# Optimization experiments

Hardware: AMD Instinct MI355X
Metric: run time of the kernel (lower is better)

## Reference

```python
import jax, jax.numpy as jnp
import numpy as np

B, T, H, L = 8, 256, 64, 3
NB, NF, HP = 17, 68, 6
K = 9  # temporal kernel
PAD = (K - 1) // 2
EPS = 1e-5


def _normalize(adj):
    adj = adj + np.eye(adj.shape[0], dtype=np.float32)
    d = adj.sum(1)
    dinv = np.power(d, -0.5)
    dinv[np.isinf(dinv)] = 0.0
    return (dinv[:, None] * adj * dinv[None, :]).astype(np.float32)


def _body_adj():
    a = np.zeros((NB, NB), np.float32)
    conns = [(0, 1), (0, 2), (1, 3), (2, 4), (0, 5), (0, 6), (5, 6), (5, 7), (7, 9), (6, 8), (8, 10), (5, 11), (6, 12), (11, 12), (11, 13), (13, 15), (12, 14), (14, 16)]
    for i, j in conns:
        a[i, j] = 1.0
        a[j, i] = 1.0
    return _normalize(a)


def _face_adj():
    a = np.zeros((NF, NF), np.float32)
    for i in range(16): a[i, i + 1] = 1.0
    for i in range(17, 21): a[i, i + 1] = 1.0
    for i in range(22, 26): a[i, i + 1] = 1.0
    for i in range(27, 30): a[i, i + 1] = 1.0
    for i in range(31, 35): a[i, i + 1] = 1.0
    for i in range(36, 41): a[i, i + 1] = 1.0
    a[41, 36] = 1.0
    for i in range(42, 47): a[i, i + 1] = 1.0
    a[47, 42] = 1.0
    for i in range(48, 59): a[i, i + 1] = 1.0
    a[59, 48] = 1.0
    for i in range(60, 67): a[i, i + 1] = 1.0
    a[67, 60] = 1.0
    a = a + a.T
    return _normalize(a)


def setup_inputs() -> dict:
    keys = iter(jax.random.split(jax.random.key(0), 80))

    def rn(shape, s):
        return jax.random.normal(next(keys), shape, jnp.float32) * s

    inp = {}
    inp['body_kps'] = jax.random.normal(next(keys), (B, T, NB * 2), jnp.float32)
    inp['face_kps_2d'] = jax.random.normal(next(keys), (B, T, NF * 2), jnp.float32)
    inp['head_pose'] = jax.random.normal(next(keys), (B, T, HP), jnp.float32)
    inp['body_adj'] = jnp.asarray(_body_adj())
    inp['face_adj'] = jnp.asarray(_face_adj())
    inp['body_proj_w'] = rn((2, H), 0.5)
    inp['body_proj_b'] = jnp.zeros((H,), jnp.float32)
    inp['face_proj_w'] = rn((2, H), 0.5)
    inp['face_proj_b'] = jnp.zeros((H,), jnp.float32)
    inp['head_w'] = rn((HP, H), 0.3)
    inp['head_b'] = jnp.zeros((H,), jnp.float32)
    for p in ('b', 'f'):
        inp[p + '_t1w'] = rn((L, H, H, K), 0.04)
        inp[p + '_t1b'] = jnp.zeros((L, H), jnp.float32)
        inp[p + '_bn1g'] = jnp.ones((L, H), jnp.float32)
        inp[p + '_bn1b'] = jnp.zeros((L, H), jnp.float32)
        inp[p + '_bn1m'] = rn((L, H), 0.1)
        inp[p + '_bn1v'] = jax.random.uniform(next(keys), (L, H), jnp.float32, 0.5, 1.5)
        inp[p + '_gcw'] = rn((L, H, H), 0.1)
        inp[p + '_gcb'] = jnp.zeros((L, H), jnp.float32)
        inp[p + '_t2w'] = rn((L, H, H, K), 0.04)
        inp[p + '_t2b'] = jnp.zeros((L, H), jnp.float32)
        inp[p + '_bn2g'] = jnp.ones((L, H), jnp.float32)
        inp[p + '_bn2b'] = jnp.zeros((L, H), jnp.float32)
        inp[p + '_bn2m'] = rn((L, H), 0.1)
        inp[p + '_bn2v'] = jax.random.uniform(next(keys), (L, H), jnp.float32, 0.5, 1.5)
    total = NB * H + NF * H + H  # 5504
    inp['fus1_w'] = rn((total, 4 * H), 0.02)
    inp['fus1_b'] = jnp.zeros((4 * H,), jnp.float32)
    inp['fus2_w'] = rn((4 * H, 2 * H), 0.06)
    inp['fus2_b'] = jnp.zeros((2 * H,), jnp.float32)
    inp['fus3_w'] = rn((2 * H, H), 0.09)
    inp['fus3_b'] = jnp.zeros((H,), jnp.float32)
    inp['fus4_w'] = rn((H, 5), 0.12)
    inp['fus4_b'] = jnp.zeros((5,), jnp.float32)
    return inp


def _conv_bn(x, w, b, g, be, m, v):
    # x: (BN, C, T); w: (O, I, K). Conv1d (pad=4) + eval-mode BatchNorm1d.
    y = jax.lax.conv_general_dilated(x, w, (1,), [(PAD, PAD)], dimension_numbers=('NCH', 'OIH', 'NCH'))
    y = y + b[None, :, None]
    inv = g * jax.lax.rsqrt(v + EPS)
    return y * inv[None, :, None] + (be - m * inv)[None, :, None]


def _block(x, adj, t1w, t1b, g1, b1, m1, v1, gw, gb, t2w, t2b, g2, b2, m2, v2):
    # x: (B, N, C, T); residual is identity (in_channels == out_channels)
    Bn, N, C, Tn = x.shape
    res = x
    h = jax.nn.relu(_conv_bn(x.reshape(Bn * N, C, Tn), t1w, t1b, g1, b1, m1, v1)).reshape(Bn, N, C, Tn)
    # spatial graph conv, batched over all timesteps at once (adj @ (x W) + b)
    support = jnp.einsum('bnct,co->bnot', h, gw)
    h = jax.nn.relu(jnp.einsum('mn,bnot->bmot', adj, support) + gb[None, None, :, None])
    h = _conv_bn(h.reshape(Bn * N, C, Tn), t2w, t2b, g2, b2, m2, v2).reshape(Bn, N, C, Tn)
    return h + res  # dropout = identity in eval


def _stream(x, n_nodes, pw, pb, adj, ps):
    Bn, Tn, _ = x.shape
    h = x.reshape(Bn, Tn, n_nodes, 2) @ pw + pb          # (B, T, N, H)
    h = jnp.transpose(h, (0, 2, 3, 1))                   # (B, N, H, T)
    for l in range(ps[0].shape[0]):
        h = _block(h, adj, *(p[l] for p in ps))
    return h.mean(axis=3).reshape(Bn, -1)                # temporal mean-pool, flatten nodes


def reference(body_kps, face_kps_2d, head_pose, body_adj, face_adj, body_proj_w, body_proj_b, face_proj_w, face_proj_b, head_w, head_b, b_t1w, b_t1b, b_bn1g, b_bn1b, b_bn1m, b_bn1v, b_gcw, b_gcb, b_t2w, b_t2b, b_bn2g, b_bn2b, b_bn2m, b_bn2v, f_t1w, f_t1b, f_bn1g, f_bn1b, f_bn1m, f_bn1v, f_gcw, f_gcb, f_t2w, f_t2b, f_bn2g, f_bn2b, f_bn2m, f_bn2v, fus1_w, fus1_b, fus2_w, fus2_b, fus3_w, fus3_b, fus4_w, fus4_b):
    bps = (b_t1w, b_t1b, b_bn1g, b_bn1b, b_bn1m, b_bn1v, b_gcw, b_gcb, b_t2w, b_t2b, b_bn2g, b_bn2b, b_bn2m, b_bn2v)
    fps = (f_t1w, f_t1b, f_bn1g, f_bn1b, f_bn1m, f_bn1v, f_gcw, f_gcb, f_t2w, f_t2b, f_bn2g, f_bn2b, f_bn2m, f_bn2v)
    bf = _stream(body_kps, NB, body_proj_w, body_proj_b, body_adj, bps)
    ff = _stream(face_kps_2d, NF, face_proj_w, face_proj_b, face_adj, fps)
    hp = jax.nn.relu(head_pose @ head_w + head_b).mean(axis=1)
    feat = jnp.concatenate([bf, ff, hp], axis=-1)
    h = jax.nn.relu(feat @ fus1_w + fus1_b)
    h = jax.nn.relu(h @ fus2_w + fus2_b)
    h = jax.nn.relu(h @ fus3_w + fus3_b)
    return h @ fus4_w + fus4_b
```

## Files before the change

kernel.cpp:

```cpp
#include <hip/hip_runtime.h>

constexpr int B_ = 8, T_ = 256, H_ = 64, L_ = 3, NB_ = 17, NF_ = 68, HP_ = 6, K_ = 9;
constexpr int FEAT_DIM = NB_ * H_ + NF_ * H_ + H_;
constexpr int HT = H_ * T_;

typedef _Float16 half4_t __attribute__((ext_vector_type(4)));
typedef _Float16 half8_t __attribute__((ext_vector_type(8)));
typedef float f32x16 __attribute__((ext_vector_type(16)));
typedef float f32x4 __attribute__((ext_vector_type(4)));

constexpr size_t SZ_AB = (size_t)B_ * NB_ * HT;
constexpr size_t SZ_AF = (size_t)B_ * NF_ * HT;
constexpr size_t OFF_TB   = 0;
constexpr size_t OFF_TF   = OFF_TB + SZ_AB / 2;
constexpr size_t OFF_SUPB = OFF_TF + SZ_AF / 2;
constexpr size_t OFF_SUPF = OFF_SUPB + SZ_AB / 2;
constexpr size_t OFF_GB   = OFF_SUPF + SZ_AF / 2;
constexpr size_t OFF_GF   = OFF_GB + SZ_AB / 2;
constexpr size_t OFF_W3   = OFF_GF + SZ_AF / 2;
constexpr size_t OFF_GW3  = OFF_W3 + 4 * 55296;
constexpr size_t OFF_B2   = OFF_GW3 + 2 * 6144;
constexpr size_t OFF_ADJPB= OFF_B2 + 768;
constexpr size_t OFF_ADJPF= OFF_ADJPB + 512;
constexpr size_t OFF_FEAT = OFF_ADJPF + 3840;
constexpr size_t OFF_P1   = OFF_FEAT + (size_t)B_ * FEAT_DIM;

struct ConvPrepSet { const float *w, *tb, *g, *bb, *m, *v; };

__global__ __launch_bounds__(256) void prep_convW_all(ConvPrepSet s0, ConvPrepSet s1,
                                                      ConvPrepSet s2, ConvPrepSet s3,
                                                      _Float16* __restrict__ w3,
                                                      float* __restrict__ b2) {
    int set = blockIdx.y;
    ConvPrepSet s = (set == 0) ? s0 : (set == 1) ? s1 : (set == 2) ? s2 : s3;
    int idx = blockIdx.x * 256 + threadIdx.x;
    int k = idx % K_; int r = idx / K_;
    int i = r % H_; r /= H_;
    int o = r % H_; int l = r / H_;
    float sc = s.g[l * H_ + o] * rsqrtf(s.v[l * H_ + o] + 1e-5f);
    w3[(size_t)set * 110592 + ((((l * K_ + k) * 8 + (i >> 3)) * H_ + o) * 8) + (i & 7)]
        = (_Float16)(s.w[idx] * sc);
    if (i == 0 && k == 0)
        b2[set * 192 + l * H_ + o] =
            s.tb[l * H_ + o] * sc + s.bb[l * H_ + o] - s.m[l * H_ + o] * sc;
}

__global__ __launch_bounds__(256) void prep_gcw_all(const float* __restrict__ g0,
                                                    const float* __restrict__ g1,
                                                    _Float16* __restrict__ w3) {
    int set = blockIdx.y;
    const float* gw = set ? g1 : g0;
    int idx = blockIdx.x * 256 + threadIdx.x;
    int o = idx % H_; int r = idx / H_;
    int c = r % H_; int l = r / H_;
    w3[(size_t)set * 12288 + (((l * 8 + (c >> 3)) * H_ + o) * 8) + (c & 7)] = (_Float16)gw[idx];
}

__global__ __launch_bounds__(256) void prep_misc(const float* __restrict__ adjB,
                                                 const float* __restrict__ adjF,
                                                 _Float16* __restrict__ pB,
                                                 _Float16* __restrict__ pF,
                                                 float* __restrict__ p1,
                                                 float* __restrict__ feat) {
    int idx = blockIdx.x * 256 + threadIdx.x;
    if (idx < 1024) {
        int m = idx >> 5, k = idx & 31;
        pB[idx] = (m < NB_ && k < NB_) ? (_Float16)adjB[m * NB_ + k] : (_Float16)0.f;
    } else if (idx < 8704) {
        int j = idx - 1024;
        int m = j / 80, k = j % 80;
        pF[j] = (m < NF_ && k < NF_) ? (_Float16)adjF[m * NF_ + k] : (_Float16)0.f;
    } else if (idx < 10752) {
        p1[idx - 8704] = 0.f;
    } else if (idx < 10752 + B_ * FEAT_DIM) {
        feat[idx - 10752] = 0.f;
    }
}

__global__ __launch_bounds__(256) void proj_kernel(const float* __restrict__ kpsB,
                                                   const float* __restrict__ pwB,
                                                   const float* __restrict__ pbB,
                                                   _Float16* __restrict__ outB,
                                                   const float* __restrict__ kpsF,
                                                   const float* __restrict__ pwF,
                                                   const float* __restrict__ pbF,
                                                   _Float16* __restrict__ outF,
                                                   const float* __restrict__ hx,
                                                   const float* __restrict__ hw,
                                                   const float* __restrict__ hb,
                                                   float* __restrict__ feat,
                                                   int nblk0, int nblk1) {
    int blk = blockIdx.x;
    if (blk >= nblk1) {
        int b = blk - nblk1;
        int c = threadIdx.x;
        if (c >= 64) return;
        float w0 = hw[c], w1 = hw[64 + c], w2 = hw[128 + c],
              w3 = hw[192 + c], w4 = hw[256 + c], w5 = hw[320 + c];
        float bias = hb[c];
        float acc = 0.f;
        for (int t = 0; t < T_; ++t) {
            const float* xr = hx + ((size_t)b * T_ + t) * HP_;
            float s = fmaf(xr[0], w0, fmaf(xr[1], w1, fmaf(xr[2], w2,
                      fmaf(xr[3], w3, fmaf(xr[4], w4, fmaf(xr[5], w5, bias))))));
            acc += fmaxf(s, 0.f);
        }
        feat[(size_t)b * FEAT_DIM + NB_ * H_ + NF_ * H_ + c] = acc * (1.f / 256.f);
        return;
    }
    const float *kps, *pw, *pb; _Float16* out; int N, bn;
    if (blk < nblk0) { kps = kpsB; pw = pwB; pb = pbB; out = outB; N = NB_; bn = blk; }
    else { kps = kpsF; pw = pwF; pb = pbF; out = outF; N = NF_; bn = blk - nblk0; }
    int b = bn / N, n = bn % N;
    int t = threadIdx.x;
    float x0 = kps[((size_t)b * T_ + t) * (N * 2) + n * 2 + 0];
    float x1 = kps[((size_t)b * T_ + t) * (N * 2) + n * 2 + 1];
    _Float16* ob = out + (size_t)bn * HT + t;
#pragma unroll 8
    for (int c = 0; c < H_; ++c)
        ob[(size_t)c * T_] = (_Float16)fmaf(x0, pw[c], fmaf(x1, pw[H_ + c], pb[c]));
}

__device__ __forceinline__ half8_t ld_b8(const _Float16* p) {
    half4_t lo = *(const half4_t*)p;
    half4_t hi = *(const half4_t*)(p + 4);
    return __builtin_shufflevector(lo, hi, 0, 1, 2, 3, 4, 5, 6, 7);
}

__device__ __forceinline__ void stage_f16(const _Float16* __restrict__ xb,
                                          _Float16* __restrict__ Xs, int tc, int tid) {
    for (int u = tid; u < 8 * 136; u += 256) {
        int oct = u / 136;
        int row = u - oct * 136;
        int t = tc * 128 + row - 4;
        _Float16 v[8];
        if (t >= 0 && t < T_) {
            const _Float16* xr = xb + (size_t)(oct * 8) * T_ + t;
#pragma unroll
            for (int j = 0; j < 8; ++j) v[j] = xr[(size_t)j * T_];
        } else {
#pragma unroll
            for (int j = 0; j < 8; ++j) v[j] = (_Float16)0.f;
        }
        _Float16* dst = &Xs[row * 68 + oct * 8];
        half4_t lo, hi;
#pragma unroll
        for (int j = 0; j < 4; ++j) { lo[j] = v[j]; hi[j] = v[4 + j]; }
        *(half4_t*)dst = lo;
        *(half4_t*)(dst + 4) = hi;
    }
}

struct CM {
    const _Float16* x; const half8_t* w1; const float* b1; const half8_t* gc; _Float16* sup;
};

__global__ __launch_bounds__(256) void convmix_kernel(CM P0, CM P1, int nblk0, int l) {
    __shared__ __align__(16) _Float16 Xs[136 * 68];
    int blk = blockIdx.x;
    CM P = (blk < nblk0) ? P0 : P1;
    if (blk >= nblk0) blk -= nblk0;
    int bn = blk >> 1, tc = blk & 1;
    int tid = threadIdx.x;
    stage_f16(P.x + (size_t)bn * HT, Xs, tc, tid);
    __syncthreads();

    int ln = tid & 63;
    int w = __builtin_amdgcn_readfirstlane(tid >> 6);
    int ln31 = ln & 31, kg = ln >> 5;
    int tsub = w * 32;

    f32x16 acc[2];
#pragma unroll
    for (int mt = 0; mt < 2; ++mt)
#pragma unroll
        for (int r = 0; r < 16; ++r) acc[mt][r] = 0.f;

    const half8_t* wl = P.w1 + (size_t)l * (K_ * 8 * H_);
    const _Float16* xrow0 = Xs + (size_t)(tsub + ln31) * 68;
#pragma unroll
    for (int tap = 0; tap < K_; ++tap) {
#pragma unroll
        for (int ks = 0; ks < 4; ++ks) {
            int i8 = ks * 2 + kg;
            half8_t a0 = wl[(tap * 8 + i8) * H_ + ln31];
            half8_t a1 = wl[(tap * 8 + i8) * H_ + 32 + ln31];
            half8_t bf = ld_b8(xrow0 + tap * 68 + i8 * 8);
            acc[0] = __builtin_amdgcn_mfma_f32_32x32x16_f16(a0, bf, acc[0], 0, 0, 0);
            acc[1] = __builtin_amdgcn_mfma_f32_32x32x16_f16(a1, bf, acc[1], 0, 0, 0);
        }
    }
    __syncthreads();

    {
        _Float16* mrow = Xs + (size_t)(4 + tsub + ln31) * 68;
#pragma unroll
        for (int mt = 0; mt < 2; ++mt) {
#pragma unroll
            for (int rg = 0; rg < 4; ++rg) {
                int o0 = mt * 32 + rg * 8 + kg * 4;
                f32x4 bv = *(const f32x4*)(P.b1 + l * H_ + o0);
                half4_t hv;
#pragma unroll
                for (int j = 0; j < 4; ++j)
                    hv[j] = (_Float16)fmaxf(acc[mt][rg * 4 + j] + bv[j], 0.f);
                *(half4_t*)(mrow + o0) = hv;
            }
        }
    }
    __syncthreads();

    f32x16 acc2[2];
#pragma unroll
    for (int mt = 0; mt < 2; ++mt)
#pragma unroll
        for (int r = 0; r < 16; ++r) acc2[mt][r] = 0.f;
    const half8_t* gl = P.gc + (size_t)l * (8 * H_);
    const _Float16* mrow = Xs + (size_t)(4 + tsub + ln31) * 68;
#pragma unroll
    for (int ks = 0; ks < 4; ++ks) {
        int i8 = ks * 2 + kg;
        half8_t a0 = gl[i8 * H_ + ln31];
        half8_t a1 = gl[i8 * H_ + 32 + ln31];
        half8_t bf = ld_b8(mrow + i8 * 8);
        acc2[0] = __builtin_amdgcn_mfma_f32_32x32x16_f16(a0, bf, acc2[0], 0, 0, 0);
        acc2[1] = __builtin_amdgcn_mfma_f32_32x32x16_f16(a1, bf, acc2[1], 0, 0, 0);
    }

    int t = tc * 128 + tsub + ln31;
    _Float16* sp = P.sup + (size_t)bn * HT + t;
#pragma unroll
    for (int mt = 0; mt < 2; ++mt) {
#pragma unroll
        for (int r = 0; r < 16; ++r) {
            int o = mt * 32 + (r & 3) + 8 * (r >> 2) + 4 * kg;
            sp[(size_t)o * T_] = (_Float16)acc2[mt][r];
        }
    }
}

struct C2 {
    const _Float16* x; const half8_t* w2; const float* b2; _Float16* trunk; int N; int fbase;
};

template <bool LAST>
__global__ __launch_bounds__(256) void conv2_kernel(C2 P0, C2 P1, int nblk0, int l,
                                                    float* __restrict__ feat) {
    __shared__ __align__(16) _Float16 Xs[136 * 68];
    int blk = blockIdx.x;
    C2 P = (blk < nblk0) ? P0 : P1;
    if (blk >= nblk0) blk -= nblk0;
    int bn = blk >> 1, tc = blk & 1;
    int tid = threadIdx.x;
    stage_f16(P.x + (size_t)bn * HT, Xs, tc, tid);
    __syncthreads();

    int ln = tid & 63;
    int w = __builtin_amdgcn_readfirstlane(tid >> 6);
    int ln31 = ln & 31, kg = ln >> 5;
    int tsub = w * 32;

    f32x16 acc[2];
#pragma unroll
    for (int mt = 0; mt < 2; ++mt)
#pragma unroll
        for (int r = 0; r < 16; ++r) acc[mt][r] = 0.f;

    const half8_t* wl = P.w2 + (size_t)l * (K_ * 8 * H_);
    const _Float16* xrow0 = Xs + (size_t)(tsub + ln31) * 68;
#pragma unroll
    for (int tap = 0; tap < K_; ++tap) {
#pragma unroll
        for (int ks = 0; ks < 4; ++ks) {
            int i8 = ks * 2 + kg;
            half8_t a0 = wl[(tap * 8 + i8) * H_ + ln31];
            half8_t a1 = wl[(tap * 8 + i8) * H_ + 32 + ln31];
            half8_t bf = ld_b8(xrow0 + tap * 68 + i8 * 8);
            acc[0] = __builtin_amdgcn_mfma_f32_32x32x16_f16(a0, bf, acc[0], 0, 0, 0);
            acc[1] = __builtin_amdgcn_mfma_f32_32x32x16_f16(a1, bf, acc[1], 0, 0, 0);
        }
    }

    int t = tc * 128 + tsub + ln31;
    const _Float16* resb = P.trunk + (size_t)bn * HT + t;
    if (!LAST) {
        _Float16* tob = P.trunk + (size_t)bn * HT + t;
#pragma unroll
        for (int mt = 0; mt < 2; ++mt) {
#pragma unroll
            for (int r = 0; r < 16; ++r) {
                int o = mt * 32 + (r & 3) + 8 * (r >> 2) + 4 * kg;
                float y = acc[mt][r] + P.b2[l * H_ + o] + (float)resb[(size_t)o * T_];
                tob[(size_t)o * T_] = (_Float16)y;
            }
        }
    } else {
        __syncthreads();
        float* red = (float*)Xs;
        float sv[2][16];
#pragma unroll
        for (int mt = 0; mt < 2; ++mt) {
#pragma unroll
            for (int r = 0; r < 16; ++r) {
                int o = mt * 32 + (r & 3) + 8 * (r >> 2) + 4 * kg;
                float s = acc[mt][r] + P.b2[l * H_ + o] + (float)resb[(size_t)o * T_];
#pragma unroll
                for (int off = 1; off < 32; off <<= 1) s += __shfl_xor(s, off);
                sv[mt][r] = s;
            }
        }
        if (ln31 == 0) {
#pragma unroll
            for (int mt = 0; mt < 2; ++mt)
#pragma unroll
                for (int r = 0; r < 16; ++r) {
                    int o = mt * 32 + (r & 3) + 8 * (r >> 2) + 4 * kg;
                    red[w * 64 + o] = sv[mt][r];
                }
        }
        __syncthreads();
        if (tid < 64) {
            float s = red[tid] + red[64 + tid] + red[128 + tid] + red[192 + tid];
            int b = bn / P.N, n = bn % P.N;
            atomicAdd(&feat[(size_t)b * FEAT_DIM + P.fbase + n * H_ + tid], s * (1.f / 256.f));
        }
    }
}

template <int N, int MT, int KS>
__device__ __forceinline__ void adjmix_impl(const _Float16* __restrict__ sup,
                                            const half8_t* __restrict__ adjP,
                                            const float* __restrict__ gb,
                                            _Float16* __restrict__ out,
                                            int blk, int l, _Float16* Ls, int tid) {
    constexpr int KP = KS * 16;
    constexpr int PITCH = KP + 4;
    int b = blk >> 7, cb = blk & 127;
    int colbase = cb * 128;
    float gbv = gb[l * H_ + (cb >> 1)];

    for (int u = tid; u < KP * 16; u += 256) {
        int n = u >> 4, cs = u & 15;
        half8_t v;
        if (n < N) v = *(const half8_t*)(sup + (size_t)(b * N + n) * HT + colbase + cs * 8);
        else {
#pragma unroll
            for (int j = 0; j < 8; ++j) v[j] = (_Float16)0.f;
        }
#pragma unroll
        for (int j = 0; j < 8; ++j) Ls[(cs * 8 + j) * PITCH + n] = v[j];
    }
    __syncthreads();

    int ln = tid & 63;
    int w = __builtin_amdgcn_readfirstlane(tid >> 6);
    int ln31 = ln & 31, kg = ln >> 5;
    int colL = w * 32 + ln31;

    f32x16 acc[MT];
#pragma unroll
    for (int mt = 0; mt < MT; ++mt)
#pragma unroll
        for (int r = 0; r < 16; ++r) acc[mt][r] = 0.f;

#pragma unroll
    for (int ks = 0; ks < KS; ++ks) {
        half8_t bf = ld_b8(&Ls[colL * PITCH + ks * 16 + kg * 8]);
#pragma unroll
        for (int mt = 0; mt < MT; ++mt) {
            half8_t af = adjP[(size_t)(mt * 32 + ln31) * (KP / 8) + ks * 2 + kg];
            acc[mt] = __builtin_amdgcn_mfma_f32_32x32x16_f16(af, bf, acc[mt], 0, 0, 0);
        }
    }

    int col = colbase + colL;
#pragma unroll
    for (int mt = 0; mt < MT; ++mt) {
#pragma unroll
        for (int r = 0; r < 16; ++r) {
            int m = mt * 32 + (r & 3) + 8 * (r >> 2) + 4 * kg;
            if (m < N)
                out[(size_t)(b * N + m) * HT + col] = (_Float16)fmaxf(acc[mt][r] + gbv, 0.f);
        }
    }
}

__global__ __launch_bounds__(256) void adjmix_kernel(
        const _Float16* __restrict__ supB, const half8_t* __restrict__ adjPB,
        const float* __restrict__ gbB, _Float16* __restrict__ outB,
        const _Float16* __restrict__ supF, const half8_t* __restrict__ adjPF,
        const float* __restrict__ gbF, _Float16* __restrict__ outF,
        int nblk0, int l) {
    __shared__ __align__(16) _Float16 Ls[128 * 84];
    int blk = blockIdx.x, tid = threadIdx.x;
    if (blk < nblk0)
        adjmix_impl<NB_, 1, 2>(supB, adjPB, gbB, outB, blk, l, Ls, tid);
    else
        adjmix_impl<NF_, 3, 5>(supF, adjPF, gbF, outF, blk - nblk0, l, Ls, tid);
}

__global__ __launch_bounds__(256) void fus1_kernel(const float* __restrict__ feat,
                                                   const float* __restrict__ w1,
                                                   float* __restrict__ p1) {
    __shared__ float fv[128];
    int b = blockIdx.x / 43, ic = blockIdx.x % 43;
    int tid = threadIdx.x;
    if (tid < 128) fv[tid] = feat[(size_t)b * FEAT_DIM + ic * 128 + tid];
    __syncthreads();
    const float* wb = w1 + (size_t)(ic * 128) * 256 + tid;
    float acc = 0.f;
#pragma unroll 4
    for (int i = 0; i < 128; ++i)
        acc = fmaf(fv[i], wb[(size_t)i * 256], acc);
    atomicAdd(&p1[b * 256 + tid], acc);
}

__global__ __launch_bounds__(256) void fus_tail_kernel(const float* __restrict__ p1,
        const float* __restrict__ b1, const float* __restrict__ w2, const float* __restrict__ b2,
        const float* __restrict__ w3, const float* __restrict__ b3,
        const float* __restrict__ w4, const float* __restrict__ b4, float* __restrict__ out) {
    __shared__ float s1[256], s2[128], s3[64];
    int b = blockIdx.x, tid = threadIdx.x;
    s1[tid] = fmaxf(p1[b * 256 + tid] + b1[tid], 0.f);
    __syncthreads();
    if (tid < 128) {
        float acc = b2[tid];
        for (int i = 0; i < 256; ++i) acc = fmaf(s1[i], w2[i * 128 + tid], acc);
        s2[tid] = fmaxf(acc, 0.f);
    }
    __syncthreads();
    if (tid < 64) {
        float acc = b3[tid];
        for (int i = 0; i < 128; ++i) acc = fmaf(s2[i], w3[i * 64 + tid], acc);
        s3[tid] = fmaxf(acc, 0.f);
    }
    __syncthreads();
    if (tid < 5) {
        float acc = b4[tid];
        for (int i = 0; i < 64; ++i) acc = fmaf(s3[i], w4[i * 5 + tid], acc);
        out[b * 5 + tid] = acc;
    }
}

extern "C" void kernel_launch(void* const* d_in, const int* in_sizes, int n_in,
                              void* d_out, int out_size, void* d_ws, size_t ws_size,
                              hipStream_t stream) {
    const float* body_kps = (const float*)d_in[0];
    const float* face_kps = (const float*)d_in[1];
    const float* head_pose = (const float*)d_in[2];
    const float* body_adj = (const float*)d_in[3];
    const float* face_adj = (const float*)d_in[4];
    const float* body_pw = (const float*)d_in[5];
    const float* body_pb = (const float*)d_in[6];
    const float* face_pw = (const float*)d_in[7];
    const float* face_pb = (const float*)d_in[8];
    const float* head_w = (const float*)d_in[9];
    const float* head_b = (const float*)d_in[10];
    const float* b_t1w = (const float*)d_in[11]; const float* b_t1b = (const float*)d_in[12];
    const float* b_g1  = (const float*)d_in[13]; const float* b_b1  = (const float*)d_in[14];
    const float* b_m1  = (const float*)d_in[15]; const float* b_v1  = (const float*)d_in[16];
    const float* b_gcw = (const float*)d_in[17]; const float* b_gcb = (const float*)d_in[18];
    const float* b_t2w = (const float*)d_in[19]; const float* b_t2b = (const float*)d_in[20];
    const float* b_g2  = (const float*)d_in[21]; const float* b_b2  = (const float*)d_in[22];
    const float* b_m2  = (const float*)d_in[23]; const float* b_v2  = (const float*)d_in[24];
    const float* f_t1w = (const float*)d_in[25]; const float* f_t1b = (const float*)d_in[26];
    const float* f_g1  = (const float*)d_in[27]; const float* f_b1  = (const float*)d_in[28];
    const float* f_m1  = (const float*)d_in[29]; const float* f_v1  = (const float*)d_in[30];
    const float* f_gcw = (const float*)d_in[31]; const float* f_gcb = (const float*)d_in[32];
    const float* f_t2w = (const float*)d_in[33]; const float* f_t2b = (const float*)d_in[34];
    const float* f_g2  = (const float*)d_in[35]; const float* f_b2  = (const float*)d_in[36];
    const float* f_m2  = (const float*)d_in[37]; const float* f_v2  = (const float*)d_in[38];
    const float* fus1_w = (const float*)d_in[39]; const float* fus1_b = (const float*)d_in[40];
    const float* fus2_w = (const float*)d_in[41]; const float* fus2_b = (const float*)d_in[42];
    const float* fus3_w = (const float*)d_in[43]; const float* fus3_b = (const float*)d_in[44];
    const float* fus4_w = (const float*)d_in[45]; const float* fus4_b = (const float*)d_in[46];

    float* ws = (float*)d_ws;
    _Float16* TrB = (_Float16*)(ws + OFF_TB);
    _Float16* TrF = (_Float16*)(ws + OFF_TF);
    _Float16* SupB = (_Float16*)(ws + OFF_SUPB);
    _Float16* SupF = (_Float16*)(ws + OFF_SUPF);
    _Float16* Gb = (_Float16*)(ws + OFF_GB);
    _Float16* Gf = (_Float16*)(ws + OFF_GF);
    _Float16* W3 = (_Float16*)(ws + OFF_W3);
    _Float16* W3b1 = W3;            _Float16* W3b2 = W3 + 110592;
    _Float16* W3f1 = W3 + 221184;   _Float16* W3f2 = W3 + 331776;
    _Float16* GW3 = (_Float16*)(ws + OFF_GW3);
    _Float16* GW3b = GW3;           _Float16* GW3f = GW3 + 12288;
    float* B2 = ws + OFF_B2;
    float* B2b1 = B2;        float* B2b2 = B2 + 192;
    float* B2f1 = B2 + 384;  float* B2f2 = B2 + 576;
    _Float16* adjPB = (_Float16*)(ws + OFF_ADJPB);
    _Float16* adjPF = (_Float16*)(ws + OFF_ADJPF);
    float* feat = ws + OFF_FEAT;
    float* p1 = ws + OFF_P1;
    float* out = (float*)d_out;

    ConvPrepSet sb1{b_t1w, b_t1b, b_g1, b_b1, b_m1, b_v1};
    ConvPrepSet sb2{b_t2w, b_t2b, b_g2, b_b2, b_m2, b_v2};
    ConvPrepSet sf1{f_t1w, f_t1b, f_g1, f_b1, f_m1, f_v1};
    ConvPrepSet sf2{f_t2w, f_t2b, f_g2, f_b2, f_m2, f_v2};
    prep_convW_all<<<dim3(432, 4), 256, 0, stream>>>(sb1, sb2, sf1, sf2, W3, B2);
    prep_gcw_all<<<dim3(48, 2), 256, 0, stream>>>(b_gcw, f_gcw, GW3);
    prep_misc<<<214, 256, 0, stream>>>(body_adj, face_adj, adjPB, adjPF, p1, feat);

    const int nB = B_ * NB_;
    const int nF = B_ * NF_;
    proj_kernel<<<nB + nF + B_, 256, 0, stream>>>(body_kps, body_pw, body_pb, TrB,
                                                  face_kps, face_pw, face_pb, TrF,
                                                  head_pose, head_w, head_b, feat,
                                                  nB, nB + nF);

    CM cmb{TrB, (const half8_t*)W3b1, B2b1, (const half8_t*)GW3b, SupB};
    CM cmf{TrF, (const half8_t*)W3f1, B2f1, (const half8_t*)GW3f, SupF};
    C2 c2b{Gb, (const half8_t*)W3b2, B2b2, TrB, NB_, 0};
    C2 c2f{Gf, (const half8_t*)W3f2, B2f2, TrF, NF_, NB_ * H_};

    const int gc = (nB + nF) * 2;
    const int n0 = nB * 2;
    const int ga = B_ * 128;

    for (int l = 0; l < L_; ++l) {
        convmix_kernel<<<gc, 256, 0, stream>>>(cmb, cmf, n0, l);
        adjmix_kernel<<<2 * ga, 256, 0, stream>>>(SupB, (const half8_t*)adjPB, b_gcb, Gb,
                                                  SupF, (const half8_t*)adjPF, f_gcb, Gf, ga, l);
        if (l < L_ - 1)
            conv2_kernel<false><<<gc, 256, 0, stream>>>(c2b, c2f, n0, l, feat);
        else
            conv2_kernel<true><<<gc, 256, 0, stream>>>(c2b, c2f, n0, l, feat);
    }

    fus1_kernel<<<B_ * 43, 256, 0, stream>>>(feat, fus1_w, p1);
    fus_tail_kernel<<<B_, 256, 0, stream>>>(p1, fus1_b, fus2_w, fus2_b, fus3_w, fus3_b,
                                            fus4_w, fus4_b, out);
}
```

Measured before the change: 395.8 us.

## Process full time axis per block in conv kernels to reuse weight fragments

Each convmix and conv2 block now covers all 256 time steps of one (batch,node) instead of half. Each wave computes two 32-step tiles, so every loaded weight fragment feeds two MFMAs, and the 4-row halo is staged once per node instead of twice. The cost is twice the LDS per block, more accumulator registers (launch bounds set to 2 blocks per SM), and half as many blocks in the grid, which lowers parallelism.

```diff
diff --git a/kernel.cpp b/kernel.cpp
--- a/kernel.cpp
+++ b/kernel.cpp
@@ -127,12 +127,12 @@
     return __builtin_shufflevector(lo, hi, 0, 1, 2, 3, 4, 5, 6, 7);
 }
 
-__device__ __forceinline__ void stage_f16(const _Float16* __restrict__ xb,
-                                          _Float16* __restrict__ Xs, int tc, int tid) {
-    for (int u = tid; u < 8 * 136; u += 256) {
-        int oct = u / 136;
-        int row = u - oct * 136;
-        int t = tc * 128 + row - 4;
+__device__ __forceinline__ void stage_full(const _Float16* __restrict__ xb,
+                                           _Float16* __restrict__ Xs, int tid) {
+    for (int u = tid; u < 8 * 264; u += 256) {
+        int oct = u / 264;
+        int row = u - oct * 264;
+        int t = row - 4;
         _Float16 v[8];
         if (t >= 0 && t < T_) {
             const _Float16* xr = xb + (size_t)(oct * 8) * T_ + t;
@@ -155,29 +155,31 @@
     const _Float16* x; const half8_t* w1; const float* b1; const half8_t* gc; _Float16* sup;
 };
 
-__global__ __launch_bounds__(256) void convmix_kernel(CM P0, CM P1, int nblk0, int l) {
-    __shared__ __align__(16) _Float16 Xs[136 * 68];
+__global__ __launch_bounds__(256, 2) void convmix_kernel(CM P0, CM P1, int nblk0, int l) {
+    __shared__ __align__(16) _Float16 Xs[264 * 68];
     int blk = blockIdx.x;
     CM P = (blk < nblk0) ? P0 : P1;
     if (blk >= nblk0) blk -= nblk0;
-    int bn = blk >> 1, tc = blk & 1;
+    int bn = blk;
     int tid = threadIdx.x;
-    stage_f16(P.x + (size_t)bn * HT, Xs, tc, tid);
+    stage_full(P.x + (size_t)bn * HT, Xs, tid);
     __syncthreads();
 
     int ln = tid & 63;
     int w = __builtin_amdgcn_readfirstlane(tid >> 6);
     int ln31 = ln & 31, kg = ln >> 5;
-    int tsub = w * 32;
-
-    f32x16 acc[2];
+    int tw = w * 64;
+
+    f32x16 acc[2][2];
 #pragma unroll
     for (int mt = 0; mt < 2; ++mt)
 #pragma unroll
-        for (int r = 0; r < 16; ++r) acc[mt][r] = 0.f;
+        for (int f = 0; f < 2; ++f)
+#pragma unroll
+            for (int r = 0; r < 16; ++r) acc[mt][f][r] = 0.f;
 
     const half8_t* wl = P.w1 + (size_t)l * (K_ * 8 * H_);
-    const _Float16* xrow0 = Xs + (size_t)(tsub + ln31) * 68;
+    const _Float16* xr0 = Xs + (size_t)(tw + ln31) * 68;
 #pragma unroll
     for (int tap = 0; tap < K_; ++tap) {
 #pragma unroll
@@ -185,56 +187,70 @@
             int i8 = ks * 2 + kg;
             half8_t a0 = wl[(tap * 8 + i8) * H_ + ln31];
             half8_t a1 = wl[(tap * 8 + i8) * H_ + 32 + ln31];
-            half8_t bf = ld_b8(xrow0 + tap * 68 + i8 * 8);
-            acc[0] = __builtin_amdgcn_mfma_f32_32x32x16_f16(a0, bf, acc[0], 0, 0, 0);
-            acc[1] = __builtin_amdgcn_mfma_f32_32x32x16_f16(a1, bf, acc[1], 0, 0, 0);
+            half8_t b0 = ld_b8(xr0 + tap * 68 + i8 * 8);
+            half8_t b1 = ld_b8(xr0 + (32 + tap) * 68 + i8 * 8);
+            acc[0][0] = __builtin_amdgcn_mfma_f32_32x32x16_f16(a0, b0, acc[0][0], 0, 0, 0);
+            acc[0][1] = __builtin_amdgcn_mfma_f32_32x32x16_f16(a0, b1, acc[0][1], 0, 0, 0);
+            acc[1][0] = __builtin_amdgcn_mfma_f32_32x32x16_f16(a1, b0, acc[1][0], 0, 0, 0);
+            acc[1][1] = __builtin_amdgcn_mfma_f32_32x32x16_f16(a1, b1, acc[1][1], 0, 0, 0);
         }
     }
     __syncthreads();
 
     {
-        _Float16* mrow = Xs + (size_t)(4 + tsub + ln31) * 68;
-#pragma unroll
-        for (int mt = 0; mt < 2; ++mt) {
-#pragma unroll
-            for (int rg = 0; rg < 4; ++rg) {
-                int o0 = mt * 32 + rg * 8 + kg * 4;
-                f32x4 bv = *(const f32x4*)(P.b1 + l * H_ + o0);
-                half4_t hv;
-#pragma unroll
-                for (int j = 0; j < 4; ++j)
-                    hv[j] = (_Float16)fmaxf(acc[mt][rg * 4 + j] + bv[j], 0.f);
-                *(half4_t*)(mrow + o0) = hv;
+#pragma unroll
+        for (int f = 0; f < 2; ++f) {
+            _Float16* mrow = Xs + (size_t)(4 + tw + f * 32 + ln31) * 68;
+#pragma unroll
+            for (int mt = 0; mt < 2; ++mt) {
+#pragma unroll
+                for (int rg = 0; rg < 4; ++rg) {
+                    int o0 = mt * 32 + rg * 8 + kg * 4;
+                    f32x4 bv = *(const f32x4*)(P.b1 + l * H_ + o0);
+                    half4_t hv;
+#pragma unroll
+                    for (int j = 0; j < 4; ++j)
+                        hv[j] = (_Float16)fmaxf(acc[mt][f][rg * 4 + j] + bv[j], 0.f);
+                    *(half4_t*)(mrow + o0) = hv;
+                }
             }
         }
     }
     __syncthreads();
 
-    f32x16 acc2[2];
+    f32x16 acc2[2][2];
 #pragma unroll
     for (int mt = 0; mt < 2; ++mt)
 #pragma unroll
-        for (int r = 0; r < 16; ++r) acc2[mt][r] = 0.f;
+        for (int f = 0; f < 2; ++f)
+#pragma unroll
+            for (int r = 0; r < 16; ++r) acc2[mt][f][r] = 0.f;
     const half8_t* gl = P.gc + (size_t)l * (8 * H_);
-    const _Float16* mrow = Xs + (size_t)(4 + tsub + ln31) * 68;
+    const _Float16* mrow0 = Xs + (size_t)(4 + tw + ln31) * 68;
 #pragma unroll
     for (int ks = 0; ks < 4; ++ks) {
         int i8 = ks * 2 + kg;
         half8_t a0 = gl[i8 * H_ + ln31];
         half8_t a1 = gl[i8 * H_ + 32 + ln31];
-        half8_t bf = ld_b8(mrow + i8 * 8);
-        acc2[0] = __builtin_amdgcn_mfma_f32_32x32x16_f16(a0, bf, acc2[0], 0, 0, 0);
-        acc2[1] = __builtin_amdgcn_mfma_f32_32x32x16_f16(a1, bf, acc2[1], 0, 0, 0);
-    }
-
-    int t = tc * 128 + tsub + ln31;
-    _Float16* sp = P.sup + (size_t)bn * HT + t;
+        half8_t b0 = ld_b8(mrow0 + i8 * 8);
+        half8_t b1 = ld_b8(mrow0 + 32 * 68 + i8 * 8);
+        acc2[0][0] = __builtin_amdgcn_mfma_f32_32x32x16_f16(a0, b0, acc2[0][0], 0, 0, 0);
+        acc2[0][1] = __builtin_amdgcn_mfma_f32_32x32x16_f16(a0, b1, acc2[0][1], 0, 0, 0);
+        acc2[1][0] = __builtin_amdgcn_mfma_f32_32x32x16_f16(a1, b0, acc2[1][0], 0, 0, 0);
+        acc2[1][1] = __builtin_amdgcn_mfma_f32_32x32x16_f16(a1, b1, acc2[1][1], 0, 0, 0);
+    }
+
+    _Float16* sp = P.sup + (size_t)bn * HT;
 #pragma unroll
     for (int mt = 0; mt < 2; ++mt) {
 #pragma unroll
-        for (int r = 0; r < 16; ++r) {
-            int o = mt * 32 + (r & 3) + 8 * (r >> 2) + 4 * kg;
-            sp[(size_t)o * T_] = (_Float16)acc2[mt][r];
+        for (int f = 0; f < 2; ++f) {
+            int t = tw + f * 32 + ln31;
+#pragma unroll
+            for (int r = 0; r < 16; ++r) {
+                int o = mt * 32 + (r & 3) + 8 * (r >> 2) + 4 * kg;
+                sp[(size_t)o * T_ + t] = (_Float16)acc2[mt][f][r];
+            }
         }
     }
 }
@@ -244,30 +260,32 @@
 };
 
 template <bool LAST>
-__global__ __launch_bounds__(256) void conv2_kernel(C2 P0, C2 P1, int nblk0, int l,
-                                                    float* __restrict__ feat) {
-    __shared__ __align__(16) _Float16 Xs[136 * 68];
+__global__ __launch_bounds__(256, 2) void conv2_kernel(C2 P0, C2 P1, int nblk0, int l,
+                                                       float* __restrict__ feat) {
+    __shared__ __align__(16) _Float16 Xs[264 * 68];
     int blk = blockIdx.x;
     C2 P = (blk < nblk0) ? P0 : P1;
     if (blk >= nblk0) blk -= nblk0;
-    int bn = blk >> 1, tc = blk & 1;
+    int bn = blk;
     int tid = threadIdx.x;
-    stage_f16(P.x + (size_t)bn * HT, Xs, tc, tid);
+    stage_full(P.x + (size_t)bn * HT, Xs, tid);
     __syncthreads();
 
     int ln = tid & 63;
     int w = __builtin_amdgcn_readfirstlane(tid >> 6);
     int ln31 = ln & 31, kg = ln >> 5;
-    int tsub = w * 32;
-
-    f32x16 acc[2];
+    int tw = w * 64;
+
+    f32x16 acc[2][2];
 #pragma unroll
     for (int mt = 0; mt < 2; ++mt)
 #pragma unroll
-        for (int r = 0; r < 16; ++r) acc[mt][r] = 0.f;
+        for (int f = 0; f < 2; ++f)
+#pragma unroll
+            for (int r = 0; r < 16; ++r) acc[mt][f][r] = 0.f;
 
     const half8_t* wl = P.w2 + (size_t)l * (K_ * 8 * H_);
-    const _Float16* xrow0 = Xs + (size_t)(tsub + ln31) * 68;
+    const _Float16* xr0 = Xs + (size_t)(tw + ln31) * 68;
 #pragma unroll
     for (int tap = 0; tap < K_; ++tap) {
 #pragma unroll
@@ -275,23 +293,29 @@
             int i8 = ks * 2 + kg;
             half8_t a0 = wl[(tap * 8 + i8) * H_ + ln31];
             half8_t a1 = wl[(tap * 8 + i8) * H_ + 32 + ln31];
-            half8_t bf = ld_b8(xrow0 + tap * 68 + i8 * 8);
-            acc[0] = __builtin_amdgcn_mfma_f32_32x32x16_f16(a0, bf, acc[0], 0, 0, 0);
-            acc[1] = __builtin_amdgcn_mfma_f32_32x32x16_f16(a1, bf, acc[1], 0, 0, 0);
-        }
-    }
-
-    int t = tc * 128 + tsub + ln31;
-    const _Float16* resb = P.trunk + (size_t)bn * HT + t;
+            half8_t b0 = ld_b8(xr0 + tap * 68 + i8 * 8);
+            half8_t b1 = ld_b8(xr0 + (32 + tap) * 68 + i8 * 8);
+            acc[0][0] = __builtin_amdgcn_mfma_f32_32x32x16_f16(a0, b0, acc[0][0], 0, 0, 0);
+            acc[0][1] = __builtin_amdgcn_mfma_f32_32x32x16_f16(a0, b1, acc[0][1], 0, 0, 0);
+            acc[1][0] = __builtin_amdgcn_mfma_f32_32x32x16_f16(a1, b0, acc[1][0], 0, 0, 0);
+            acc[1][1] = __builtin_amdgcn_mfma_f32_32x32x16_f16(a1, b1, acc[1][1], 0, 0, 0);
+        }
+    }
+
+    const _Float16* resb = P.trunk + (size_t)bn * HT;
     if (!LAST) {
-        _Float16* tob = P.trunk + (size_t)bn * HT + t;
+        _Float16* tob = P.trunk + (size_t)bn * HT;
 #pragma unroll
         for (int mt = 0; mt < 2; ++mt) {
 #pragma unroll
-            for (int r = 0; r < 16; ++r) {
-                int o = mt * 32 + (r & 3) + 8 * (r >> 2) + 4 * kg;
-                float y = acc[mt][r] + P.b2[l * H_ + o] + (float)resb[(size_t)o * T_];
-                tob[(size_t)o * T_] = (_Float16)y;
+            for (int f = 0; f < 2; ++f) {
+                int t = tw + f * 32 + ln31;
+#pragma unroll
+                for (int r = 0; r < 16; ++r) {
+                    int o = mt * 32 + (r & 3) + 8 * (r >> 2) + 4 * kg;
+                    float y = acc[mt][f][r] + P.b2[l * H_ + o] + (float)resb[(size_t)o * T_ + t];
+                    tob[(size_t)o * T_ + t] = (_Float16)y;
+                }
             }
         }
     } else {
@@ -303,7 +327,9 @@
 #pragma unroll
             for (int r = 0; r < 16; ++r) {
                 int o = mt * 32 + (r & 3) + 8 * (r >> 2) + 4 * kg;
-                float s = acc[mt][r] + P.b2[l * H_ + o] + (float)resb[(size_t)o * T_];
+                float b2v = P.b2[l * H_ + o];
+                float s = (acc[mt][0][r] + b2v + (float)resb[(size_t)o * T_ + tw + ln31])
+                        + (acc[mt][1][r] + b2v + (float)resb[(size_t)o * T_ + tw + 32 + ln31]);
 #pragma unroll
                 for (int off = 1; off < 32; off <<= 1) s += __shfl_xor(s, off);
                 sv[mt][r] = s;
@@ -516,8 +542,8 @@
     C2 c2b{Gb, (const half8_t*)W3b2, B2b2, TrB, NB_, 0};
     C2 c2f{Gf, (const half8_t*)W3f2, B2f2, TrF, NF_, NB_ * H_};
 
-    const int gc = (nB + nF) * 2;
-    const int n0 = nB * 2;
+    const int gc = nB + nF;
+    const int n0 = nB;
     const int ga = B_ * 128;
 
     for (int l = 0; l < L_; ++l) {
```

Result: no change. 394.0 us (-0.5%).
